# Optimization experiments

Measured on AMD Instinct MI355X. Metric: run time of the kernel, lower is better.

Reference implementation:

```python
import jax, jax.numpy as jnp
import numpy as np
import math

D_MODEL = 256
N_HEAD = 1
C_IN = 32
B, L = 8, 2048
FACTOR = 5


def _pos_encoding(L, D):
    pos = jnp.arange(L, dtype=jnp.float32)[:, None]
    div = jnp.exp(jnp.arange(0, D, 2, dtype=jnp.float32) * (-math.log(10000.0) / D))
    pe = jnp.zeros((L, D), dtype=jnp.float32)
    pe = pe.at[:, 0::2].set(jnp.sin(pos * div))
    pe = pe.at[:, 1::2].set(jnp.cos(pos * div))
    return pe


def _layer_norm(x, g, b, eps=1e-5):
    mu = x.mean(-1, keepdims=True)
    var = ((x - mu) ** 2).mean(-1, keepdims=True)
    return (x - mu) / jnp.sqrt(var + eps) * g + b


def setup_inputs():
    key = jax.random.key(0)
    ks = jax.random.split(key, 16)
    D = D_MODEL
    s = 0.02
    p = {}
    p["x"] = jax.random.normal(ks[0], (B, L, C_IN), jnp.float32)
    sample_k = min(FACTOR * math.ceil(math.log(L)), L)  # = 40 for L=2048
    p["sample_idx"] = jax.random.randint(ks[1], (L, sample_k), 0, L)
    p["emb_w"] = jax.random.normal(ks[2], (C_IN, N_HEAD * D)) * s
    p["emb_b"] = jnp.zeros((N_HEAD * D,))
    for i, n in enumerate(["wq", "wk", "wv", "wo"]):
        p[n] = jax.random.normal(ks[3 + i], (D, D)) * s
        p["b" + n[1]] = jnp.zeros((D,))
    p["conv1_w"] = jax.random.normal(ks[7], (D, D)) * s  # Conv1d kernel=1 == linear, d_ff = d_model
    p["conv1_b"] = jnp.zeros((D,))
    p["conv2_w"] = jax.random.normal(ks[8], (D, D)) * s
    p["conv2_b"] = jnp.zeros((D,))
    for n in ["ln1", "ln2", "lnf"]:
        p[n + "_g"] = jnp.ones((D,))
        p[n + "_b"] = jnp.zeros((D,))
    p["gru_wih"] = jax.random.normal(ks[9], (3 * D, D)) * s
    p["gru_whh"] = jax.random.normal(ks[10], (3 * D, D)) * s
    p["gru_bih"] = jnp.zeros((3 * D,))
    p["gru_bhh"] = jnp.zeros((3 * D,))
    p["fc_w"] = jax.random.normal(ks[11], (D, 1)) * s
    p["fc_b"] = jnp.zeros((1,))
    return p


def _forward(x, sample_idx, emb_w, emb_b, wq, bq, wk, bk, wv, bv, wo, bo,
             conv1_w, conv1_b, conv2_w, conv2_b, ln1_g, ln1_b, ln2_g, ln2_b,
             lnf_g, lnf_b, gru_wih, gru_whh, gru_bih, gru_bhh, fc_w, fc_b):
    Bx, Lx, _ = x.shape
    H = N_HEAD
    src = x @ emb_w + emb_b + _pos_encoding(Lx, emb_w.shape[1])  # [B,L,D]
    D = src.shape[-1]
    dk = D // H

    def heads(t, w, b):
        return (t @ w + b).reshape(Bx, Lx, H, dk).transpose(0, 2, 1, 3)  # [B,H,L,dk]

    Q = heads(src, wq, bq)
    K = heads(src, wk, bk)
    V = heads(src, wv, bv)

    # ---- ProbSparse attention (Informer, non-masked) ----
    u = sample_idx.shape[1]                                  # n_top == sample_k here
    K_sample = K[:, :, sample_idx, :]                        # [B,H,L,s,dk]
    QK_s = jnp.einsum("bhld,bhlsd->bhls", Q, K_sample)
    M = QK_s.max(-1) - QK_s.sum(-1) / Lx                     # sparsity measure per query
    _, top = jax.lax.top_k(M, u)                             # [B,H,u]
    Q_red = jnp.take_along_axis(Q, top[..., None], axis=2)   # [B,H,u,dk]
    scores = jnp.einsum("bhud,bhkd->bhuk", Q_red, K) / jnp.sqrt(jnp.float32(dk))
    attn = jax.nn.softmax(scores, axis=-1)
    upd = jnp.einsum("bhuk,bhkd->bhud", attn, V)             # [B,H,u,dk]
    ctx = jnp.broadcast_to(V.mean(axis=2, keepdims=True), Q.shape)  # initial context = mean(V)
    bi = jnp.arange(Bx)[:, None, None]
    hi = jnp.arange(H)[None, :, None]
    ctx = ctx.at[bi, hi, top].set(upd)
    out = ctx.transpose(0, 2, 1, 3).reshape(Bx, Lx, D) @ wo + bo

    # ---- EncoderLayer FFN (Conv1d k=1 -> gelu -> Conv1d k=1), residuals, norms ----
    x1 = _layer_norm(src + out, ln1_g, ln1_b)
    y = jax.nn.gelu(x1 @ conv1_w + conv1_b, approximate=False)
    y = y @ conv2_w + conv2_b
    enc = _layer_norm(_layer_norm(x1 + y, ln2_g, ln2_b), lnf_g, lnf_b)

    # ---- GRU: faithful to source bug: seq-major nn.GRU fed [B,L,D] -> scans over batch dim ----
    def step(h, xt):
        gi = xt @ gru_wih.T + gru_bih
        gh = h @ gru_whh.T + gru_bhh
        ir, iz, inn = jnp.split(gi, 3, axis=-1)
        hr, hz, hn = jnp.split(gh, 3, axis=-1)
        r = jax.nn.sigmoid(ir + hr)
        z = jax.nn.sigmoid(iz + hz)
        n = jnp.tanh(inn + r * hn)
        h = (1.0 - z) * n + z * h
        return h, h

    h0 = jnp.zeros((Lx, enc.shape[-1]), enc.dtype)
    _, gru_out = jax.lax.scan(step, h0, enc)  # [B,L,D]
    return gru_out[:, -1, :] @ fc_w + fc_b    # [B,1]


def reference(x, sample_idx, emb_w, emb_b, wq, bq, wk, bk, wv, bv, wo, bo,
              conv1_w, conv1_b, conv2_w, conv2_b, ln1_g, ln1_b, ln2_g, ln2_b,
              lnf_g, lnf_b, gru_wih, gru_whh, gru_bih, gru_bhh, fc_w, fc_b):
    return _forward(x, sample_idx, emb_w, emb_b, wq, bq, wk, bk, wv, bv, wo, bo,
                    conv1_w, conv1_b, conv2_w, conv2_b, ln1_g, ln1_b, ln2_g, ln2_b,
                    lnf_g, lnf_b, gru_wih, gru_whh, gru_bih, gru_bhh, fc_w, fc_b)
```

## Files before the change

### kernel.cpp

```cpp
#include <hip/hip_runtime.h>
#include <hip/hip_bf16.h>
#include <math.h>

#define BB 8
#define LL 2048
#define CIN 32
#define DD 256
#define UU 40
#define NROW (BB*LL)
#define NSL  (NROW*DD)
#define GB 8

typedef unsigned short u16;
typedef __attribute__((ext_vector_type(8))) short short8;
typedef __attribute__((ext_vector_type(4))) float f32x4;

__device__ __forceinline__ u16 f2bf(float v) {
    unsigned u = __float_as_uint(v);
    unsigned r = (u + 0x7FFF + ((u >> 16) & 1)) >> 16;
    return (u16)r;
}
__device__ __forceinline__ float bf2f(u16 h) {
    return __uint_as_float(((unsigned)h) << 16);
}

template<int CTRL>
__device__ __forceinline__ float dpp_add(float v) {
    int s = __builtin_amdgcn_update_dpp(0, __float_as_int(v), CTRL, 0xf, 0xf, true);
    return v + __int_as_float(s);
}
__device__ __forceinline__ float row16_sum(float v) {
    v = dpp_add<0x118>(v);
    v = dpp_add<0x114>(v);
    v = dpp_add<0x112>(v);
    v = dpp_add<0x111>(v);
    return v;
}
__device__ __forceinline__ float dot4(float4 a, float4 b) {
    return a.x * b.x + a.y * b.y + a.z * b.z + a.w * b.w;
}

__global__ __launch_bounds__(256) void src_kernel(
    const float* __restrict__ x, const float* __restrict__ emb_w,
    const float* __restrict__ emb_b,
    u16* __restrict__ srch, u16* __restrict__ srcl, float* __restrict__ srcrow)
{
    __shared__ float xs[CIN];
    const int orig = blockIdx.x;
    const int b = orig & 7;
    const int l = orig >> 3;
    const int r = (b << 11) | l;
    const int d = threadIdx.x;
    if (d < CIN) xs[d] = x[(size_t)r * CIN + d];
    __syncthreads();
    float acc = emb_b[d];
#pragma unroll 8
    for (int c = 0; c < CIN; ++c) acc += xs[c] * emb_w[c * DD + d];
    const int i = d >> 1;
    const float ang = (float)l * expf((float)(2 * i) * (-9.210340371976184f / 256.0f));
    const float pe = (d & 1) ? cosf(ang) : sinf(ang);
    const float v = acc + pe;
    const u16 h = f2bf(v);
    srch[(size_t)r * DD + d] = h;
    srcl[(size_t)r * DD + d] = f2bf(v - bf2f(h));
    if (l == LL - 1) srcrow[b * DD + d] = v;
}

__global__ __launch_bounds__(256) void splitw_kernel(
    const float* __restrict__ wq, const float* __restrict__ wk,
    const float* __restrict__ wv, u16* __restrict__ whT, u16* __restrict__ wlT)
{
    const int o = blockIdx.x, n = blockIdx.y, k = threadIdx.x;
    const float* W = (o == 0) ? wq : (o == 1) ? wk : wv;
    const float v = W[(size_t)k * DD + n];
    const u16 h = f2bf(v);
    whT[((size_t)o << 16) + n * DD + k] = h;
    wlT[((size_t)o << 16) + n * DD + k] = f2bf(v - bf2f(h));
}

__global__ __launch_bounds__(256) void gemm_kv_mfma(
    const u16* __restrict__ srch, const u16* __restrict__ srcl,
    const u16* __restrict__ whT, const u16* __restrict__ wlT,
    const float* __restrict__ bk, const float* __restrict__ bv,
    float* __restrict__ K, float* __restrict__ V)
{
    __shared__ __align__(16) u16 AhS[64][40], AlS[64][40], BhS[64][40], BlS[64][40];
    const int t = threadIdx.x;
    const int bx = blockIdx.x;
    const int mt = (bx & 7) * 32 + (bx >> 3);
    const int bm = mt * 64;
    const int bn = blockIdx.y * 64;
    const int o  = blockIdx.z + 1;
    const u16* wh = whT + ((size_t)o << 16);
    const u16* wl = wlT + ((size_t)o << 16);
    const float* bias = (o == 1) ? bk : bv;
    float* C = (o == 1) ? K : V;

    const int srow = t >> 2, sk8 = (t & 3) * 8;
    const int lane = t & 63, w = t >> 6;
    const int frow = lane & 15, kg = (lane >> 4) * 8;

    f32x4 acc[4];
#pragma unroll
    for (int nf = 0; nf < 4; ++nf) acc[nf] = (f32x4){0.f, 0.f, 0.f, 0.f};

    for (int ks = 0; ks < 8; ++ks) {
        const int kb = ks * 32 + sk8;
        *(short8*)&AhS[srow][sk8] = *(const short8*)&srch[(size_t)(bm + srow) * DD + kb];
        *(short8*)&AlS[srow][sk8] = *(const short8*)&srcl[(size_t)(bm + srow) * DD + kb];
        *(short8*)&BhS[srow][sk8] = *(const short8*)&wh[(size_t)(bn + srow) * DD + kb];
        *(short8*)&BlS[srow][sk8] = *(const short8*)&wl[(size_t)(bn + srow) * DD + kb];
        __syncthreads();
        const short8 ah = *(const short8*)&AhS[w * 16 + frow][kg];
        const short8 al = *(const short8*)&AlS[w * 16 + frow][kg];
#pragma unroll
        for (int nf = 0; nf < 4; ++nf) {
            const short8 bh = *(const short8*)&BhS[nf * 16 + frow][kg];
            const short8 bl = *(const short8*)&BlS[nf * 16 + frow][kg];
            acc[nf] = __builtin_amdgcn_mfma_f32_16x16x32_bf16(al, bh, acc[nf], 0, 0, 0);
            acc[nf] = __builtin_amdgcn_mfma_f32_16x16x32_bf16(ah, bl, acc[nf], 0, 0, 0);
            acc[nf] = __builtin_amdgcn_mfma_f32_16x16x32_bf16(ah, bh, acc[nf], 0, 0, 0);
        }
        __syncthreads();
    }
#pragma unroll
    for (int nf = 0; nf < 4; ++nf) {
#pragma unroll
        for (int r = 0; r < 4; ++r) {
            const int row = bm + w * 16 + (lane >> 4) * 4 + r;
            const int col = bn + nf * 16 + (lane & 15);
            C[(size_t)row * DD + col] = acc[nf][r] + bias[col];
        }
    }
}

__global__ __launch_bounds__(256) void gemm_q_qks(
    const u16* __restrict__ srch, const u16* __restrict__ srcl,
    const u16* __restrict__ whT, const u16* __restrict__ wlT,
    const float* __restrict__ bq, const float* __restrict__ Kf,
    const int* __restrict__ sidx,
    float* __restrict__ qrow, float* __restrict__ M)
{
    __shared__ __align__(16) u16 AhS[64][40], AlS[64][40];
    __shared__ __align__(16) u16 BhS[256][40], BlS[256][40];
    __shared__ __align__(16) float qS[64][260];
    __shared__ int sidxS[64 * UU];
    __shared__ float qkS[64][41];

    const int t = threadIdx.x;
    const int bx = blockIdx.x;
    const int b  = bx & 7;
    const int mtb = bx >> 3;
    const int l0 = mtb * 64;
    const size_t gr0 = ((size_t)b << 11) + l0;

    const int srow = t >> 2, sk8 = (t & 3) * 8;
    const int lane = t & 63, w = t >> 6;
    const int frow = lane & 15, kg = (lane >> 4) * 8;

    f32x4 acc[16];
#pragma unroll
    for (int nf = 0; nf < 16; ++nf) acc[nf] = (f32x4){0.f, 0.f, 0.f, 0.f};

    for (int ks = 0; ks < 8; ++ks) {
        const int kb = ks * 32 + sk8;
        *(short8*)&AhS[srow][sk8] = *(const short8*)&srch[(gr0 + srow) * DD + kb];
        *(short8*)&AlS[srow][sk8] = *(const short8*)&srcl[(gr0 + srow) * DD + kb];
#pragma unroll
        for (int i = 0; i < 4; ++i) {
            const int br = srow + 64 * i;
            *(short8*)&BhS[br][sk8] = *(const short8*)&whT[(size_t)br * DD + kb];
            *(short8*)&BlS[br][sk8] = *(const short8*)&wlT[(size_t)br * DD + kb];
        }
        __syncthreads();
        const short8 ah = *(const short8*)&AhS[w * 16 + frow][kg];
        const short8 al = *(const short8*)&AlS[w * 16 + frow][kg];
#pragma unroll
        for (int nf = 0; nf < 16; ++nf) {
            const short8 bh = *(const short8*)&BhS[nf * 16 + frow][kg];
            const short8 bl = *(const short8*)&BlS[nf * 16 + frow][kg];
            acc[nf] = __builtin_amdgcn_mfma_f32_16x16x32_bf16(al, bh, acc[nf], 0, 0, 0);
            acc[nf] = __builtin_amdgcn_mfma_f32_16x16x32_bf16(ah, bl, acc[nf], 0, 0, 0);
            acc[nf] = __builtin_amdgcn_mfma_f32_16x16x32_bf16(ah, bh, acc[nf], 0, 0, 0);
        }
        __syncthreads();
    }
#pragma unroll
    for (int nf = 0; nf < 16; ++nf) {
        const int col = nf * 16 + (lane & 15);
        const float bcol = bq[col];
#pragma unroll
        for (int r = 0; r < 4; ++r) {
            const int row = w * 16 + (lane >> 4) * 4 + r;
            qS[row][col] = acc[nf][r] + bcol;
        }
    }
    for (int i = t; i < 64 * UU; i += 256) sidxS[i] = sidx[l0 * UU + i];
    __syncthreads();

    if (mtb == 31) qrow[b * DD + t] = qS[63][t];

    const float* Kb = Kf + ((size_t)b << 11) * DD;
    const int g = t >> 4, j = t & 15;
#pragma unroll
    for (int i = 0; i < 4; ++i) {
        const int row = g + 16 * i;
        const float4* q4 = (const float4*)&qS[row][j * 16];
        const float4 q0 = q4[0], q1 = q4[1], q2 = q4[2], q3 = q4[3];
        for (int s = 0; s < UU; ++s) {
            const int idx = sidxS[row * UU + s];
            const float4* kr = (const float4*)&Kb[(size_t)idx * DD];
            float d = dot4(q0, kr[j * 4 + 0]) + dot4(q1, kr[j * 4 + 1])
                    + dot4(q2, kr[j * 4 + 2]) + dot4(q3, kr[j * 4 + 3]);
            d = row16_sum(d);
            if (j == 15) qkS[row][s] = d;
        }
    }
    __syncthreads();
    if (t < 64) {
        float mx = -1e30f, sm = 0.0f;
#pragma unroll
        for (int s = 0; s < UU; ++s) { float v = qkS[t][s]; mx = fmaxf(mx, v); sm += v; }
        M[gr0 + t] = mx - sm * (1.0f / (float)LL);
    }
}

__global__ __launch_bounds__(256) void rank_kernel(
    const float* __restrict__ M, int* __restrict__ flag)
{
    __shared__ int redi[256];
    const int b = blockIdx.x, t = threadIdx.x;
    const float* Mb = M + (size_t)b * LL;
    const float ref = Mb[LL - 1];
    int cnt = 0;
    for (int l = t; l < LL; l += 256)
        if (l != LL - 1 && Mb[l] >= ref) cnt++;
    redi[t] = cnt; __syncthreads();
    for (int s = 128; s; s >>= 1) { if (t < s) redi[t] += redi[t + s]; __syncthreads(); }
    if (t == 0) flag[b] = (redi[0] < UU) ? 1 : 0;
}

__global__ __launch_bounds__(256) void ctx_scores(
    const float* __restrict__ qrow, const float* __restrict__ K,
    const int* __restrict__ flag, float* __restrict__ sc)
{
    const int b = blockIdx.x;
    if (!flag[b]) return;
    const int t = threadIdx.x, grp = t >> 4, j = t & 15;
    const size_t base = (size_t)b * LL * DD;
    const float4* qr = (const float4*)&qrow[b * DD];
    const float4 q0 = qr[j * 4 + 0], q1 = qr[j * 4 + 1],
                 q2 = qr[j * 4 + 2], q3 = qr[j * 4 + 3];
    const int k0 = blockIdx.y * 128 + grp * 8;
#pragma unroll
    for (int i = 0; i < 8; ++i) {
        const int k = k0 + i;
        const float4* kr = (const float4*)&K[base + (size_t)k * DD];
        float d = dot4(q0, kr[j * 4 + 0]) + dot4(q1, kr[j * 4 + 1])
                + dot4(q2, kr[j * 4 + 2]) + dot4(q3, kr[j * 4 + 3]);
        d = row16_sum(d);
        if (j == 15) sc[b * LL + k] = d * (1.0f / 16.0f);
    }
}

__global__ __launch_bounds__(256) void ctx_softmax(
    const int* __restrict__ flag, float* __restrict__ sc, float* __restrict__ ssum)
{
    __shared__ float red[256];
    const int b = blockIdx.x;
    if (!flag[b]) return;
    const int t = threadIdx.x;
    float* s = sc + b * LL;
    float lm = -1e30f;
    for (int k = t; k < LL; k += 256) lm = fmaxf(lm, s[k]);
    red[t] = lm; __syncthreads();
    for (int st = 128; st; st >>= 1) { if (t < st) red[t] = fmaxf(red[t], red[t + st]); __syncthreads(); }
    const float mx = red[0]; __syncthreads();
    float ls = 0.0f;
    for (int k = t; k < LL; k += 256) { float e = expf(s[k] - mx); s[k] = e; ls += e; }
    red[t] = ls; __syncthreads();
    for (int st = 128; st; st >>= 1) { if (t < st) red[t] += red[t + st]; __syncthreads(); }
    if (t == 0) ssum[b] = red[0];
}

__global__ __launch_bounds__(256) void ctx_pv(
    const float* __restrict__ V, const float* __restrict__ sc,
    const int* __restrict__ flag, float* __restrict__ part)
{
    const int b = blockIdx.x, slice = blockIdx.y;
    const int d = threadIdx.x;
    const size_t base = (size_t)b * LL * DD;
    const int k0 = slice * 256;
    float acc = 0.0f;
    if (flag[b]) {
#pragma unroll 4
        for (int k = k0; k < k0 + 256; ++k)
            acc += sc[b * LL + k] * V[base + (size_t)k * DD + d];
    } else {
#pragma unroll 4
        for (int k = k0; k < k0 + 256; ++k)
            acc += V[base + (size_t)k * DD + d];
    }
    part[(b * 8 + slice) * DD + d] = acc;
}

__device__ __forceinline__ float block_sum256(float v, float* red) {
    const int t = threadIdx.x;
    __syncthreads();
    red[t] = v; __syncthreads();
    for (int s = 128; s; s >>= 1) { if (t < s) red[t] += red[t + s]; __syncthreads(); }
    return red[0];
}

__global__ __launch_bounds__(256) void tail_kernel(
    const float* __restrict__ srcrow, const float* __restrict__ part,
    const float* __restrict__ ssum, const int* __restrict__ flag,
    const float* __restrict__ wo, const float* __restrict__ bo,
    const float* __restrict__ c1w, const float* __restrict__ c1b,
    const float* __restrict__ c2w, const float* __restrict__ c2b,
    const float* __restrict__ g1, const float* __restrict__ b1,
    const float* __restrict__ g2, const float* __restrict__ b2,
    const float* __restrict__ gf, const float* __restrict__ bf,
    float* __restrict__ enc)
{
    __shared__ float xs[DD];
    __shared__ float red[DD];
    const int b = blockIdx.x, d = threadIdx.x;

    float cv = 0.0f;
#pragma unroll
    for (int i = 0; i < 8; ++i) cv += part[(b * 8 + i) * DD + d];
    cv = flag[b] ? cv / ssum[b] : cv * (1.0f / (float)LL);

    xs[d] = cv; __syncthreads();
    float o = bo[d];
    for (int j = 0; j < DD; ++j) o += xs[j] * wo[j * DD + d];
    const float v = srcrow[b * DD + d] + o;

    float mu = block_sum256(v, red) * (1.0f / DD);
    float dv = v - mu;
    float var = block_sum256(dv * dv, red) * (1.0f / DD);
    const float x1 = dv * rsqrtf(var + 1e-5f) * g1[d] + b1[d];

    __syncthreads(); xs[d] = x1; __syncthreads();
    float a = c1b[d];
    for (int j = 0; j < DD; ++j) a += xs[j] * c1w[j * DD + d];
    a = 0.5f * a * (1.0f + erff(a * 0.70710678118654752f));

    __syncthreads(); xs[d] = a; __syncthreads();
    float y = c2b[d];
    for (int j = 0; j < DD; ++j) y += xs[j] * c2w[j * DD + d];

    float t2 = x1 + y;
    mu = block_sum256(t2, red) * (1.0f / DD);
    dv = t2 - mu;
    var = block_sum256(dv * dv, red) * (1.0f / DD);
    float t3 = dv * rsqrtf(var + 1e-5f) * g2[d] + b2[d];

    mu = block_sum256(t3, red) * (1.0f / DD);
    dv = t3 - mu;
    var = block_sum256(dv * dv, red) * (1.0f / DD);
    enc[b * DD + d] = dv * rsqrtf(var + 1e-5f) * gf[d] + bf[d];
}

__global__ __launch_bounds__(768) void gru_coop_kernel(
    const float* __restrict__ enc, const float* __restrict__ wih,
    const float* __restrict__ whh, const float* __restrict__ bih,
    const float* __restrict__ bhh, const float* __restrict__ fcw,
    const float* __restrict__ fcb,
    unsigned long long* __restrict__ hpub,
    float* __restrict__ out)
{
    __shared__ float whhS[96][257];
    __shared__ float encS[BB][260];
    __shared__ float giS[96][8];
    __shared__ float hS[DD];
    __shared__ float ghS[96];
    __shared__ float red[256];
    const int g = blockIdx.x, t = threadIdx.x;

#pragma unroll
    for (int i = 0; i < 8; ++i) {
        const int f4 = t + 768 * i;
        const int lr = f4 >> 6, c4 = f4 & 63;
        const int R = (lr >> 5) * 256 + g * 32 + (lr & 31);
        const float4 w = *(const float4*)&whh[(size_t)R * DD + c4 * 4];
        whhS[lr][c4 * 4 + 0] = w.x; whhS[lr][c4 * 4 + 1] = w.y;
        whhS[lr][c4 * 4 + 2] = w.z; whhS[lr][c4 * 4 + 3] = w.w;
    }
    for (int e = t; e < BB * DD; e += 768) encS[e >> 8][e & 255] = enc[e];
    if (t < DD) hS[t] = 0.0f;
    __syncthreads();

    {
        const int lr = t >> 3, b = t & 7;
        const int R = (lr >> 5) * 256 + g * 32 + (lr & 31);
        float acc = bih[R];
        const float4* w4 = (const float4*)&wih[(size_t)R * DD];
#pragma unroll 8
        for (int jc = 0; jc < 64; ++jc) {
            const float4 w = w4[jc];
            acc += encS[b][jc * 4 + 0] * w.x + encS[b][jc * 4 + 1] * w.y
                 + encS[b][jc * 4 + 2] * w.z + encS[b][jc * 4 + 3] * w.w;
        }
        giS[lr][b] = acc;
    }
    __syncthreads();

    for (int step = 1; step <= BB; ++step) {
        const int b = step - 1;
        const int lr = t >> 3, s = t & 7;
        float p = 0.0f;
#pragma unroll
        for (int k = 0; k < 32; ++k) {
            const int c = s * 32 + ((k + s * 4) & 31);
            p += whhS[lr][c] * hS[c];
        }
        p = dpp_add<0x114>(p); p = dpp_add<0x112>(p); p = dpp_add<0x111>(p);
        if (s == 7) ghS[lr] = p + bhh[(lr >> 5) * 256 + g * 32 + (lr & 31)];
        __syncthreads();

        if (t < 32) {
            const float r  = 1.0f / (1.0f + expf(-(giS[t][b]      + ghS[t])));
            const float z  = 1.0f / (1.0f + expf(-(giS[32 + t][b] + ghS[32 + t])));
            const float n  = tanhf(giS[64 + t][b] + r * ghS[64 + t]);
            const float hnew = (1.0f - z) * n + z * hS[g * 32 + t];
            const unsigned long long w =
                ((unsigned long long)(unsigned)step << 32) | (unsigned long long)__float_as_uint(hnew);
            __hip_atomic_store(&hpub[g * 32 + t], w, __ATOMIC_RELAXED, __HIP_MEMORY_SCOPE_AGENT);
        }
        __syncthreads();
        if (t < DD) {
            unsigned long long w;
            do {
                w = __hip_atomic_load(&hpub[t], __ATOMIC_RELAXED, __HIP_MEMORY_SCOPE_AGENT);
            } while ((int)(w >> 32) != step);
            hS[t] = __uint_as_float((unsigned)w);
        }
        __syncthreads();

        if (g == 0) {
            if (t < DD) red[t] = hS[t] * fcw[t];
            __syncthreads();
            for (int st2 = 128; st2; st2 >>= 1) { if (t < st2) red[t] += red[t + st2]; __syncthreads(); }
            if (t == 0) out[b] = red[0] + fcb[0];
            __syncthreads();
        }
    }
}

extern "C" void kernel_launch(void* const* d_in, const int* in_sizes, int n_in,
                              void* d_out, int out_size, void* d_ws, size_t ws_size,
                              hipStream_t stream)
{
    const float* x      = (const float*)d_in[0];
    const int*   sidx   = (const int*)  d_in[1];
    const float* emb_w  = (const float*)d_in[2];
    const float* emb_b  = (const float*)d_in[3];
    const float* wq     = (const float*)d_in[4];
    const float* bq     = (const float*)d_in[5];
    const float* wk     = (const float*)d_in[6];
    const float* bk     = (const float*)d_in[7];
    const float* wv     = (const float*)d_in[8];
    const float* bv     = (const float*)d_in[9];
    const float* wo     = (const float*)d_in[10];
    const float* bo     = (const float*)d_in[11];
    const float* c1w    = (const float*)d_in[12];
    const float* c1b    = (const float*)d_in[13];
    const float* c2w    = (const float*)d_in[14];
    const float* c2b    = (const float*)d_in[15];
    const float* ln1g   = (const float*)d_in[16];
    const float* ln1b   = (const float*)d_in[17];
    const float* ln2g   = (const float*)d_in[18];
    const float* ln2b   = (const float*)d_in[19];
    const float* lnfg   = (const float*)d_in[20];
    const float* lnfb   = (const float*)d_in[21];
    const float* wih    = (const float*)d_in[22];
    const float* whh    = (const float*)d_in[23];
    const float* bih    = (const float*)d_in[24];
    const float* bhh    = (const float*)d_in[25];
    const float* fcw    = (const float*)d_in[26];
    const float* fcb    = (const float*)d_in[27];

    float* ws  = (float*)d_ws;
    float* K    = ws;
    float* V    = K + NSL;
    float* Mv   = V + NSL;
    int*   flag = (int*)(Mv + NROW);
    float* sc   = (float*)(flag + 16);
    float* ssum = sc + BB * LL;
    float* part = ssum + 16;
    float* srcrow = part + BB * 8 * DD;
    float* qrow = srcrow + BB * DD;
    float* enc  = qrow + BB * DD;
    unsigned long long* hpub = (unsigned long long*)(enc + BB * DD);
    u16* srch = (u16*)(hpub + 256);
    u16* srcl = srch + NSL;
    u16* whT  = srcl + NSL;
    u16* wlT  = whT + 3 * 65536;

    hipMemsetAsync(hpub, 0, 256 * sizeof(unsigned long long), stream);

    splitw_kernel<<<dim3(3, 256), 256, 0, stream>>>(wq, wk, wv, whT, wlT);
    src_kernel<<<NROW, 256, 0, stream>>>(x, emb_w, emb_b, srch, srcl, srcrow);
    gemm_kv_mfma<<<dim3(256, 4, 2), 256, 0, stream>>>(srch, srcl, whT, wlT,
                                                      bk, bv, K, V);
    gemm_q_qks<<<256, 256, 0, stream>>>(srch, srcl, whT, wlT, bq, K, sidx,
                                        qrow, Mv);
    rank_kernel<<<BB, 256, 0, stream>>>(Mv, flag);
    ctx_scores<<<dim3(BB, 16), 256, 0, stream>>>(qrow, K, flag, sc);
    ctx_softmax<<<BB, 256, 0, stream>>>(flag, sc, ssum);
    ctx_pv<<<dim3(BB, 8), 256, 0, stream>>>(V, sc, flag, part);
    tail_kernel<<<BB, 256, 0, stream>>>(srcrow, part, ssum, flag, wo, bo,
                                        c1w, c1b, c2w, c2b,
                                        ln1g, ln1b, ln2g, ln2b, lnfg, lnfb, enc);
    gru_coop_kernel<<<GB, 768, 0, stream>>>(enc, wih, whh, bih, bhh, fcw, fcb,
                                            hpub, (float*)d_out);
}
```

Before: 199.6 us.

## Unfuse Q projection into QKV GEMM and add separate sampled QK kernel

Q is now computed by the same 64x64-tiled GEMM as K and V, with a third z-slice, and written to a new global Qf buffer. The sampled Q·K scoring moves into a separate lightweight kernel that launches one wave per query row. Before, a fused kernel ran only 256 blocks, each with a very large LDS footprint. The aim is higher parallelism and occupancy for both the Q GEMM and the gather-dot phase, at the cost of writing and re-reading a 16 MB Q tensor and one extra launch.

```diff
diff --git a/kernel.cpp b/kernel.cpp
--- a/kernel.cpp
+++ b/kernel.cpp
@@ -78,11 +78,13 @@
     wlT[((size_t)o << 16) + n * DD + k] = f2bf(v - bf2f(h));
 }
 
-__global__ __launch_bounds__(256) void gemm_kv_mfma(
+__global__ __launch_bounds__(256) void gemm_qkv_mfma(
     const u16* __restrict__ srch, const u16* __restrict__ srcl,
     const u16* __restrict__ whT, const u16* __restrict__ wlT,
-    const float* __restrict__ bk, const float* __restrict__ bv,
-    float* __restrict__ K, float* __restrict__ V)
+    const float* __restrict__ bq, const float* __restrict__ bk,
+    const float* __restrict__ bv,
+    float* __restrict__ Qf, float* __restrict__ K, float* __restrict__ V,
+    float* __restrict__ qrow)
 {
     __shared__ __align__(16) u16 AhS[64][40], AlS[64][40], BhS[64][40], BlS[64][40];
     const int t = threadIdx.x;
@@ -90,11 +92,11 @@
     const int mt = (bx & 7) * 32 + (bx >> 3);
     const int bm = mt * 64;
     const int bn = blockIdx.y * 64;
-    const int o  = blockIdx.z + 1;
+    const int o  = blockIdx.z;
     const u16* wh = whT + ((size_t)o << 16);
     const u16* wl = wlT + ((size_t)o << 16);
-    const float* bias = (o == 1) ? bk : bv;
-    float* C = (o == 1) ? K : V;
+    const float* bias = (o == 0) ? bq : (o == 1) ? bk : bv;
+    float* C = (o == 0) ? Qf : (o == 1) ? K : V;
 
     const int srow = t >> 2, sk8 = (t & 3) * 8;
     const int lane = t & 63, w = t >> 6;
@@ -129,99 +131,51 @@
         for (int r = 0; r < 4; ++r) {
             const int row = bm + w * 16 + (lane >> 4) * 4 + r;
             const int col = bn + nf * 16 + (lane & 15);
-            C[(size_t)row * DD + col] = acc[nf][r] + bias[col];
-        }
-    }
-}
-
-__global__ __launch_bounds__(256) void gemm_q_qks(
-    const u16* __restrict__ srch, const u16* __restrict__ srcl,
-    const u16* __restrict__ whT, const u16* __restrict__ wlT,
-    const float* __restrict__ bq, const float* __restrict__ Kf,
-    const int* __restrict__ sidx,
-    float* __restrict__ qrow, float* __restrict__ M)
-{
-    __shared__ __align__(16) u16 AhS[64][40], AlS[64][40];
-    __shared__ __align__(16) u16 BhS[256][40], BlS[256][40];
-    __shared__ __align__(16) float qS[64][260];
-    __shared__ int sidxS[64 * UU];
-    __shared__ float qkS[64][41];
-
+            const float v = acc[nf][r] + bias[col];
+            C[(size_t)row * DD + col] = v;
+            if (o == 0 && (row & (LL - 1)) == (LL - 1))
+                qrow[(row >> 11) * DD + col] = v;
+        }
+    }
+}
+
+__global__ __launch_bounds__(256) void qks_probe(
+    const float* __restrict__ Qf, const float* __restrict__ Kf,
+    const int* __restrict__ sidx, float* __restrict__ M)
+{
+    __shared__ float qk[4][UU];
+    const int bid = blockIdx.x;
+    const int b = bid & 7;
+    const int grp = bid >> 3;
     const int t = threadIdx.x;
-    const int bx = blockIdx.x;
-    const int b  = bx & 7;
-    const int mtb = bx >> 3;
-    const int l0 = mtb * 64;
-    const size_t gr0 = ((size_t)b << 11) + l0;
-
-    const int srow = t >> 2, sk8 = (t & 3) * 8;
-    const int lane = t & 63, w = t >> 6;
-    const int frow = lane & 15, kg = (lane >> 4) * 8;
-
-    f32x4 acc[16];
-#pragma unroll
-    for (int nf = 0; nf < 16; ++nf) acc[nf] = (f32x4){0.f, 0.f, 0.f, 0.f};
-
-    for (int ks = 0; ks < 8; ++ks) {
-        const int kb = ks * 32 + sk8;
-        *(short8*)&AhS[srow][sk8] = *(const short8*)&srch[(gr0 + srow) * DD + kb];
-        *(short8*)&AlS[srow][sk8] = *(const short8*)&srcl[(gr0 + srow) * DD + kb];
-#pragma unroll
-        for (int i = 0; i < 4; ++i) {
-            const int br = srow + 64 * i;
-            *(short8*)&BhS[br][sk8] = *(const short8*)&whT[(size_t)br * DD + kb];
-            *(short8*)&BlS[br][sk8] = *(const short8*)&wlT[(size_t)br * DD + kb];
-        }
-        __syncthreads();
-        const short8 ah = *(const short8*)&AhS[w * 16 + frow][kg];
-        const short8 al = *(const short8*)&AlS[w * 16 + frow][kg];
-#pragma unroll
-        for (int nf = 0; nf < 16; ++nf) {
-            const short8 bh = *(const short8*)&BhS[nf * 16 + frow][kg];
-            const short8 bl = *(const short8*)&BlS[nf * 16 + frow][kg];
-            acc[nf] = __builtin_amdgcn_mfma_f32_16x16x32_bf16(al, bh, acc[nf], 0, 0, 0);
-            acc[nf] = __builtin_amdgcn_mfma_f32_16x16x32_bf16(ah, bl, acc[nf], 0, 0, 0);
-            acc[nf] = __builtin_amdgcn_mfma_f32_16x16x32_bf16(ah, bh, acc[nf], 0, 0, 0);
-        }
-        __syncthreads();
-    }
-#pragma unroll
-    for (int nf = 0; nf < 16; ++nf) {
-        const int col = nf * 16 + (lane & 15);
-        const float bcol = bq[col];
-#pragma unroll
-        for (int r = 0; r < 4; ++r) {
-            const int row = w * 16 + (lane >> 4) * 4 + r;
-            qS[row][col] = acc[nf][r] + bcol;
-        }
-    }
-    for (int i = t; i < 64 * UU; i += 256) sidxS[i] = sidx[l0 * UU + i];
+    const int wv = t >> 6;
+    const int lane = t & 63;
+    const int sub = lane >> 4;
+    const int j = lane & 15;
+    const int l = grp * 4 + wv;
+    const size_t r = ((size_t)b << 11) + l;
+
+    const float4* q4 = (const float4*)&Qf[r * DD];
+    const float4 q0 = q4[j * 4 + 0], q1 = q4[j * 4 + 1],
+                 q2 = q4[j * 4 + 2], q3 = q4[j * 4 + 3];
+    const float* Kb = Kf + ((size_t)b << 11) * DD;
+    const int* si = sidx + (size_t)l * UU;
+
+#pragma unroll 2
+    for (int s0 = 0; s0 < UU; s0 += 4) {
+        const int idx = si[s0 + sub];
+        const float4* kr = (const float4*)&Kb[(size_t)idx * DD];
+        float d = dot4(q0, kr[j * 4 + 0]) + dot4(q1, kr[j * 4 + 1])
+                + dot4(q2, kr[j * 4 + 2]) + dot4(q3, kr[j * 4 + 3]);
+        d = row16_sum(d);
+        if (j == 15) qk[wv][s0 + sub] = d;
+    }
     __syncthreads();
-
-    if (mtb == 31) qrow[b * DD + t] = qS[63][t];
-
-    const float* Kb = Kf + ((size_t)b << 11) * DD;
-    const int g = t >> 4, j = t & 15;
-#pragma unroll
-    for (int i = 0; i < 4; ++i) {
-        const int row = g + 16 * i;
-        const float4* q4 = (const float4*)&qS[row][j * 16];
-        const float4 q0 = q4[0], q1 = q4[1], q2 = q4[2], q3 = q4[3];
-        for (int s = 0; s < UU; ++s) {
-            const int idx = sidxS[row * UU + s];
-            const float4* kr = (const float4*)&Kb[(size_t)idx * DD];
-            float d = dot4(q0, kr[j * 4 + 0]) + dot4(q1, kr[j * 4 + 1])
-                    + dot4(q2, kr[j * 4 + 2]) + dot4(q3, kr[j * 4 + 3]);
-            d = row16_sum(d);
-            if (j == 15) qkS[row][s] = d;
-        }
-    }
-    __syncthreads();
-    if (t < 64) {
+    if (t < 4) {
         float mx = -1e30f, sm = 0.0f;
 #pragma unroll
-        for (int s = 0; s < UU; ++s) { float v = qkS[t][s]; mx = fmaxf(mx, v); sm += v; }
-        M[gr0 + t] = mx - sm * (1.0f / (float)LL);
+        for (int s = 0; s < UU; ++s) { float v = qk[t][s]; mx = fmaxf(mx, v); sm += v; }
+        M[((size_t)b << 11) + grp * 4 + t] = mx - sm * (1.0f / (float)LL);
     }
 }
 
@@ -498,15 +452,15 @@
     u16* srcl = srch + NSL;
     u16* whT  = srcl + NSL;
     u16* wlT  = whT + 3 * 65536;
+    float* Qf = (float*)(wlT + 3 * 65536);
 
     hipMemsetAsync(hpub, 0, 256 * sizeof(unsigned long long), stream);
 
     splitw_kernel<<<dim3(3, 256), 256, 0, stream>>>(wq, wk, wv, whT, wlT);
     src_kernel<<<NROW, 256, 0, stream>>>(x, emb_w, emb_b, srch, srcl, srcrow);
-    gemm_kv_mfma<<<dim3(256, 4, 2), 256, 0, stream>>>(srch, srcl, whT, wlT,
-                                                      bk, bv, K, V);
-    gemm_q_qks<<<256, 256, 0, stream>>>(srch, srcl, whT, wlT, bq, K, sidx,
-                                        qrow, Mv);
+    gemm_qkv_mfma<<<dim3(256, 4, 3), 256, 0, stream>>>(srch, srcl, whT, wlT,
+                                                       bq, bk, bv, Qf, K, V, qrow);
+    qks_probe<<<NROW / 4, 256, 0, stream>>>(Qf, K, sidx, Mv);
     rank_kernel<<<BB, 256, 0, stream>>>(Mv, flag);
     ctx_scores<<<dim3(BB, 16), 256, 0, stream>>>(qrow, K, flag, sc);
     ctx_softmax<<<BB, 256, 0, stream>>>(flag, sc, ssum);
```

Result: faster. 191.9 us (-3.9%).
